# Kernel optimization log

Measured on AMD Instinct MI355X. Metric: run time of the kernel, lower is better.

## Reference

```python
import jax, jax.numpy as jnp
import numpy as np
import math

B, T, D_MODEL, N_HEAD = 2, 2048, 1024, 16
NUM_BUCKETS, MAX_DIST = 32, 128
D_HEAD = D_MODEL // N_HEAD


def _relative_position_bucket(rel_pos, num_buckets=NUM_BUCKETS, max_distance=MAX_DIST):
    # bidirectional=True branch of the torch code
    nb = num_buckets // 2
    buckets = (rel_pos > 0).astype(jnp.int32) * nb
    rel_pos = jnp.abs(rel_pos)
    max_exact = nb // 2
    is_small = rel_pos < max_exact
    # guard log(0); masked out by is_small anyway
    large = max_exact + (
        jnp.log(jnp.maximum(rel_pos, 1).astype(jnp.float32) / max_exact)
        / math.log(max_distance / max_exact) * (nb - max_exact)
    ).astype(jnp.int32)
    large = jnp.minimum(large, nb - 1)
    return buckets + jnp.where(is_small, rel_pos, large)


def compute_bias(rel_bias, q_len, kv_len):
    qp = jnp.arange(q_len, dtype=jnp.int32)[:, None]
    kp = jnp.arange(kv_len, dtype=jnp.int32)[None, :]
    buckets = _relative_position_bucket(kp - qp)          # [Tq, Tkv]
    vals = rel_bias[buckets]                              # [Tq, Tkv, H]
    return jnp.transpose(vals, (2, 0, 1))                 # [H, Tq, Tkv]


def setup_inputs() -> dict:
    key = jax.random.key(0)
    ks = jax.random.split(key, 9)
    inp = {
        'q': jax.random.normal(ks[0], (B, T, D_MODEL), jnp.float32),
        'k': jax.random.normal(ks[1], (B, T, D_MODEL), jnp.float32),
        'v': jax.random.normal(ks[2], (B, T, D_MODEL), jnp.float32),
        'mask': jax.random.randint(ks[3], (B, T, T), 0, 2, jnp.int32),
        'Wq': jax.random.normal(ks[4], (D_MODEL, D_MODEL), jnp.float32) * 0.02,
        'Wk': jax.random.normal(ks[5], (D_MODEL, D_MODEL), jnp.float32) * 0.02,
        'Wv': jax.random.normal(ks[6], (D_MODEL, D_MODEL), jnp.float32) * 0.02,
        'Wfc': jax.random.normal(ks[7], (D_MODEL, D_MODEL), jnp.float32) * 0.02,
        'rel_bias': jax.random.normal(ks[8], (NUM_BUCKETS, N_HEAD), jnp.float32) * 0.02,
    }
    return inp


def reference(q, k, v, mask, Wq, Wk, Wv, Wfc, rel_bias):
    b, tq, _ = q.shape
    tkv = k.shape[1]
    qh = (q @ Wq).reshape(b, tq, N_HEAD, D_HEAD)
    kh = (k @ Wk).reshape(b, tkv, N_HEAD, D_HEAD)
    vh = (v @ Wv).reshape(b, tkv, N_HEAD, D_HEAD)
    attn = jnp.einsum('blhd,bthd->bhlt', qh, kh) / np.sqrt(D_HEAD).astype(np.float32)
    position_bias = compute_bias(rel_bias, tq, tkv)       # [H, Tq, Tkv]
    attn = attn + position_bias[None]                     # broadcast over batch
    attn = jnp.where(mask[:, None] == 0, -1e9, attn)
    attn = jax.nn.softmax(attn, axis=-1)                  # dropout: eval mode (identity)
    out = jnp.einsum('bhlt,bthd->blhd', attn, vh).reshape(b, tq, D_MODEL)
    out = out @ Wfc
    return out, position_bias[:, None]                    # bias returned as [H,1,Tq,Tkv] like torch
```

## Files before the change

kernel.cpp:

```cpp
#include <hip/hip_runtime.h>
#include <math.h>

#define TT 2048
#define BB 2
#define HH 16
#define DMODEL 1024
#define NREL 4095

typedef __attribute__((ext_vector_type(8)))  _Float16 half8;
typedef __attribute__((ext_vector_type(4)))  _Float16 half4;
typedef __attribute__((ext_vector_type(16))) float    f32x16;
typedef __attribute__((ext_vector_type(4)))  int      int4v;

#define EXP2F(x) __builtin_amdgcn_exp2f(x)

__device__ __forceinline__ f32x16 zero16() {
    f32x16 v;
#pragma unroll
    for (int i = 0; i < 16; ++i) v[i] = 0.f;
    return v;
}

__device__ __forceinline__ unsigned pkh(float a, float b) {
    union { _Float16 h[2]; unsigned u; } x;
    x.h[0] = (_Float16)a; x.h[1] = (_Float16)b;
    return x.u;
}

__device__ __forceinline__ void gload16(const void* g, void* l) {
    __builtin_amdgcn_global_load_lds(
        (const __attribute__((address_space(1))) void*)g,
        (__attribute__((address_space(3))) void*)l, 16, 0, 0);
}

__device__ __forceinline__ int rel_bucket(int rel) {
    int base = rel > 0 ? 16 : 0;
    int r = rel < 0 ? -rel : rel;
    int lb;
    if (r < 8)       lb = r;
    else if (r < 12) lb = 8;
    else if (r < 16) lb = 9;
    else if (r < 23) lb = 10;
    else if (r < 32) lb = 11;
    else if (r < 46) lb = 12;
    else if (r < 64) lb = 13;
    else if (r < 91) lb = 14;
    else             lb = 15;
    return base + lb;
}

__global__ __launch_bounds__(256) void prep_kernel(
    const float* __restrict__ q, const float* __restrict__ k,
    const float* __restrict__ v, const int* __restrict__ mask,
    const float* __restrict__ W0, const float* __restrict__ W1,
    const float* __restrict__ W2, const float* __restrict__ W3,
    const float* __restrict__ rel_bias,
    _Float16* __restrict__ q16, _Float16* __restrict__ k16,
    _Float16* __restrict__ v16, _Float16* __restrict__ WT,
    float* __restrict__ btable, unsigned* __restrict__ mb)
{
    __shared__ float t[64][65];
    int bid = blockIdx.x, tid = threadIdx.x;
    if (bid < 256) {
        int idx = bid * 256 + tid;
        if (idx < HH * NREL) {
            int h = idx / NREL, ri = idx % NREL;
            btable[idx] = rel_bias[rel_bucket(ri - (TT - 1)) * HH + h];
        }
    } else if (bid < 1280) {
        int zz = (bid - 256) >> 8, inner = (bid - 256) & 255;
        const float* src = zz == 0 ? W0 : zz == 1 ? W1 : zz == 2 ? W2 : W3;
        _Float16* dst = WT + (size_t)zz * DMODEL * DMODEL;
        int k0 = (inner >> 4) * 64, n0 = (inner & 15) * 64;
        int r = tid >> 4, c4 = (tid & 15) * 4;
#pragma unroll
        for (int i = 0; i < 4; ++i) {
            float4 vv = *(const float4*)(src + (size_t)(k0 + r + 16 * i) * DMODEL + n0 + c4);
            t[r + 16 * i][c4] = vv.x; t[r + 16 * i][c4 + 1] = vv.y;
            t[r + 16 * i][c4 + 2] = vv.z; t[r + 16 * i][c4 + 3] = vv.w;
        }
        __syncthreads();
        int rn = tid >> 2, ck = (tid & 3) * 16;
        half8 h0, h1;
#pragma unroll
        for (int j = 0; j < 8; ++j) h0[j] = (_Float16)t[ck + j][rn];
#pragma unroll
        for (int j = 0; j < 8; ++j) h1[j] = (_Float16)t[ck + 8 + j][rn];
        *(half8*)(dst + (size_t)(n0 + rn) * DMODEL + k0 + ck) = h0;
        *(half8*)(dst + (size_t)(n0 + rn) * DMODEL + k0 + ck + 8) = h1;
    } else if (bid < 7424) {
        int zz = (bid - 1280) >> 11, inner = (bid - 1280) & 2047;
        const float* src = zz == 0 ? q : zz == 1 ? k : v;
        _Float16* dst = zz == 0 ? q16 : zz == 1 ? k16 : v16;
        int i = inner * 256 + tid;
        const float4* in4 = (const float4*)src;
        float4 v0 = in4[(size_t)i * 2], v1 = in4[(size_t)i * 2 + 1];
        half8 h = {(_Float16)v0.x, (_Float16)v0.y, (_Float16)v0.z, (_Float16)v0.w,
                   (_Float16)v1.x, (_Float16)v1.y, (_Float16)v1.z, (_Float16)v1.w};
        *(half8*)(dst + (size_t)i * 8) = h;
    } else {
        int g = (bid - 7424) * 256 + tid;
        int vv = mask[g];
        unsigned long long bal = __ballot(vv != 0);
        if ((g & 63) == 0) {
            int word = g >> 5;
            mb[word]     = (unsigned)bal;
            mb[word + 1] = (unsigned)(bal >> 32);
        }
    }
}

__global__ __launch_bounds__(256) void gemm_proj3(
    const _Float16* __restrict__ q16, const _Float16* __restrict__ k16,
    const _Float16* __restrict__ v16, const _Float16* __restrict__ WT,
    _Float16* __restrict__ qhf, _Float16* __restrict__ khf,
    _Float16* __restrict__ vtf, int zbase)
{
    __shared__ __align__(16) char lds[65536];
    int z = zbase + blockIdx.z;
    const _Float16* A  = z == 0 ? q16 : z == 1 ? k16 : v16;
    const _Float16* Bt = WT + (size_t)z * DMODEL * DMODEL;
    int bm = blockIdx.x * 128, bn = blockIdx.y * 128;
    int tid = threadIdx.x;
    int wv = tid >> 6, lane = tid & 63, hi = lane >> 5;
    int lo = lane & 31;
    int wr = wv >> 1, wc = wv & 1;
    int srow = wv * 32 + (lane >> 3);
    int scol = (lane & 7) * 8;
    const _Float16* Abase = A  + (size_t)(bm + srow) * DMODEL + scol;
    const _Float16* Bbase = Bt + (size_t)(bn + srow) * DMODEL + scol;

    f32x16 acc[2][2];
    acc[0][0] = zero16(); acc[0][1] = zero16();
    acc[1][0] = zero16(); acc[1][1] = zero16();

    auto stage = [&](int buf, int kt) {
#pragma unroll
        for (int t = 0; t < 4; ++t) {
            gload16(Abase + (size_t)t * 8 * DMODEL + kt * 64, lds + buf + wv * 4096 + t * 1024);
            gload16(Bbase + (size_t)t * 8 * DMODEL + kt * 64, lds + buf + 16384 + wv * 4096 + t * 1024);
        }
    };
    auto compute = [&](int buf) {
#pragma unroll
        for (int kk = 0; kk < 4; ++kk) {
            int cs = 2 * kk + hi;
            half8 a[2], b[2];
#pragma unroll
            for (int i = 0; i < 2; ++i) {
                a[i] = *(const half8*)(lds + buf + (wr * 64 + i * 32 + lo) * 128 + cs * 16);
                b[i] = *(const half8*)(lds + buf + 16384 + (wc * 64 + i * 32 + lo) * 128 + cs * 16);
            }
            acc[0][0] = __builtin_amdgcn_mfma_f32_32x32x16_f16(a[0], b[0], acc[0][0], 0, 0, 0);
            acc[0][1] = __builtin_amdgcn_mfma_f32_32x32x16_f16(a[0], b[1], acc[0][1], 0, 0, 0);
            acc[1][0] = __builtin_amdgcn_mfma_f32_32x32x16_f16(a[1], b[0], acc[1][0], 0, 0, 0);
            acc[1][1] = __builtin_amdgcn_mfma_f32_32x32x16_f16(a[1], b[1], acc[1][1], 0, 0, 0);
        }
    };

    stage(0, 0);
    __syncthreads();
    for (int kt = 0; kt < 16; kt += 2) {
        stage(32768, kt + 1);
        compute(0);
        __syncthreads();
        stage(0, kt + 2 < 16 ? kt + 2 : 15);
        compute(32768);
        __syncthreads();
    }

    if (z < 2) {
        _Float16* C = z == 0 ? qhf : khf;
#pragma unroll
        for (int j = 0; j < 2; ++j) {
            int n = bn + wc * 64 + j * 32 + lo;
            int h = n >> 6, d = n & 63;
#pragma unroll
            for (int i = 0; i < 2; ++i) {
                int mb2 = bm + wr * 64 + i * 32 + 4 * hi;
#pragma unroll
                for (int r = 0; r < 16; ++r) {
                    int m = mb2 + (r & 3) + 8 * (r >> 2);
                    int b = m >> 11, t = m & (TT - 1);
                    C[((size_t)(b * HH + h) * TT + t) * 64 + d] = (_Float16)acc[i][j][r];
                }
            }
        }
    } else {
#pragma unroll
        for (int j = 0; j < 2; ++j) {
            int n = bn + wc * 64 + j * 32 + lo;
            int h = n >> 6, d = n & 63;
#pragma unroll
            for (int i = 0; i < 2; ++i) {
                int mb2 = bm + wr * 64 + i * 32 + 4 * hi;
                int b = mb2 >> 11, tb = mb2 & (TT - 1);
#pragma unroll
                for (int r4 = 0; r4 < 4; ++r4) {
                    half4 hv = {(_Float16)acc[i][j][4 * r4 + 0], (_Float16)acc[i][j][4 * r4 + 1],
                                (_Float16)acc[i][j][4 * r4 + 2], (_Float16)acc[i][j][4 * r4 + 3]};
                    *(half4*)(vtf + ((size_t)(b * HH + h) * 64 + d) * TT + tb + 8 * r4) = hv;
                }
            }
        }
    }
}

__global__ __launch_bounds__(256) void attn_mfma(
    const _Float16* __restrict__ qh, const _Float16* __restrict__ kh,
    const _Float16* __restrict__ vt, const unsigned* __restrict__ maskbits,
    const float* __restrict__ btable, _Float16* __restrict__ Oout)
{
    __shared__ float bias_lds[4096];
    int bid = blockIdx.x;
    int xcd = bid & 7, j = bid >> 3;
    int qt = j & 15, bh = xcd + 8 * (j >> 4);
    int h = bh & 15, b = bh >> 4;
    int tid = threadIdx.x;
    int wv = tid >> 6, lane = tid & 63, lo = lane & 31, hi = lane >> 5;
    int q0 = qt * 128 + wv * 32;

    {
        const float* bsrc = btable + h * NREL;
#pragma unroll
        for (int i = 0; i < 16; ++i) {
            int idx = i * 256 + tid;
            bias_lds[idx] = bsrc[idx < NREL ? idx : NREL - 1] * 1.44269504f;
        }
    }

    const size_t bhoff = (size_t)(b * HH + h);
    const _Float16* Q = qh + (bhoff * TT + q0) * 64;
    const _Float16* K = kh + bhoff * TT * 64;
    const _Float16* V = vt + bhoff * 64 * TT;

    half8 qf[4];
#pragma unroll
    for (int c = 0; c < 4; ++c)
        qf[c] = *(const half8*)(Q + (size_t)lo * 64 + c * 16 + hi * 8);

    const int bofs = (TT - 1) - (q0 + lo) + 4 * hi;
    const unsigned* mw = maskbits + ((size_t)b * TT + q0 + lo) * 64;
    const float SC = 0.125f * 1.44269504f;

    f32x16 acco0 = zero16(), acco1 = zero16();
    float m = -INFINITY, l = 0.f;

    __syncthreads();

    for (int kt = 0; kt < 16; ++kt) {
        int k0 = kt * 128;
        unsigned wmA0 = mw[4 * kt], wmA1 = mw[4 * kt + 1];
        unsigned wmB0 = mw[4 * kt + 2], wmB1 = mw[4 * kt + 3];

        f32x16 sA0 = zero16(), sA1 = zero16(), sB0 = zero16(), sB1 = zero16();
        {
            half8 kf[4];
#pragma unroll
            for (int c = 0; c < 4; ++c)
                kf[c] = *(const half8*)(K + (size_t)(k0 + lo) * 64 + c * 16 + hi * 8);
            __builtin_amdgcn_s_setprio(1);
#pragma unroll
            for (int c = 0; c < 4; ++c)
                sA0 = __builtin_amdgcn_mfma_f32_32x32x16_f16(kf[c], qf[c], sA0, 0, 0, 0);
            __builtin_amdgcn_s_setprio(0);
#pragma unroll
            for (int c = 0; c < 4; ++c)
                kf[c] = *(const half8*)(K + (size_t)(k0 + 32 + lo) * 64 + c * 16 + hi * 8);
            __builtin_amdgcn_s_setprio(1);
#pragma unroll
            for (int c = 0; c < 4; ++c)
                sA1 = __builtin_amdgcn_mfma_f32_32x32x16_f16(kf[c], qf[c], sA1, 0, 0, 0);
            __builtin_amdgcn_s_setprio(0);
#pragma unroll
            for (int c = 0; c < 4; ++c)
                kf[c] = *(const half8*)(K + (size_t)(k0 + 64 + lo) * 64 + c * 16 + hi * 8);
            __builtin_amdgcn_s_setprio(1);
#pragma unroll
            for (int c = 0; c < 4; ++c)
                sB0 = __builtin_amdgcn_mfma_f32_32x32x16_f16(kf[c], qf[c], sB0, 0, 0, 0);
            __builtin_amdgcn_s_setprio(0);
#pragma unroll
            for (int c = 0; c < 4; ++c)
                kf[c] = *(const half8*)(K + (size_t)(k0 + 96 + lo) * 64 + c * 16 + hi * 8);
            __builtin_amdgcn_s_setprio(1);
#pragma unroll
            for (int c = 0; c < 4; ++c)
                sB1 = __builtin_amdgcn_mfma_f32_32x32x16_f16(kf[c], qf[c], sB1, 0, 0, 0);
            __builtin_amdgcn_s_setprio(0);
        }

        unsigned wsA0 = wmA0 >> (hi * 4), wsA1 = wmA1 >> (hi * 4);
        unsigned wsB0 = wmB0 >> (hi * 4), wsB1 = wmB1 >> (hi * 4);
        int bbase = bofs + k0;
#pragma unroll
        for (int r = 0; r < 16; ++r) {
            int sh = (r & 3) + 8 * (r >> 2);
            float a0 = fmaf(sA0[r], SC, bias_lds[bbase + sh]);
            float a1 = fmaf(sA1[r], SC, bias_lds[bbase + sh + 32]);
            float b0 = fmaf(sB0[r], SC, bias_lds[bbase + sh + 64]);
            float b1 = fmaf(sB1[r], SC, bias_lds[bbase + sh + 96]);
            sA0[r] = ((wsA0 >> sh) & 1) ? a0 : -1e9f;
            sA1[r] = ((wsA1 >> sh) & 1) ? a1 : -1e9f;
            sB0[r] = ((wsB0 >> sh) & 1) ? b0 : -1e9f;
            sB1[r] = ((wsB1 >> sh) & 1) ? b1 : -1e9f;
        }

        float tr[8];
#pragma unroll
        for (int r = 0; r < 8; ++r) {
            float x0 = fmaxf(fmaxf(sA0[r], sA0[r + 8]), fmaxf(sA1[r], sA1[r + 8]));
            float x1 = fmaxf(fmaxf(sB0[r], sB0[r + 8]), fmaxf(sB1[r], sB1[r + 8]));
            tr[r] = fmaxf(x0, x1);
        }
#pragma unroll
        for (int r = 0; r < 4; ++r) tr[r] = fmaxf(tr[r], tr[r + 4]);
        float tm = fmaxf(fmaxf(tr[0], tr[1]), fmaxf(tr[2], tr[3]));
        tm = fmaxf(tm, __shfl_xor(tm, 32));
        float mnew = fmaxf(m, tm);
        float corr = EXP2F(m - mnew);
        m = mnew;

#pragma unroll
        for (int r = 0; r < 16; ++r) sA0[r] = EXP2F(sA0[r] - m);
#pragma unroll
        for (int r = 0; r < 16; ++r) sA1[r] = EXP2F(sA1[r] - m);
#pragma unroll
        for (int r = 0; r < 16; ++r) sB0[r] = EXP2F(sB0[r] - m);
#pragma unroll
        for (int r = 0; r < 16; ++r) sB1[r] = EXP2F(sB1[r] - m);
#pragma unroll
        for (int r = 0; r < 8; ++r)
            tr[r] = ((sA0[r] + sA0[r + 8]) + (sA1[r] + sA1[r + 8]))
                  + ((sB0[r] + sB0[r + 8]) + (sB1[r] + sB1[r + 8]));
#pragma unroll
        for (int r = 0; r < 4; ++r) tr[r] += tr[r + 4];
        float rs = (tr[0] + tr[1]) + (tr[2] + tr[3]);
        rs += __shfl_xor(rs, 32);
        l = l * corr + rs;
#pragma unroll
        for (int r = 0; r < 16; ++r) { acco0[r] *= corr; acco1[r] *= corr; }

        half8 pbA[4], pbB[4];
#pragma unroll
        for (int g = 0; g < 2; ++g)
#pragma unroll
            for (int hc = 0; hc < 2; ++hc) {
                int r0 = hc * 8;
                float p0 = g ? sA1[r0 + 0] : sA0[r0 + 0];
                float p1 = g ? sA1[r0 + 1] : sA0[r0 + 1];
                float p2 = g ? sA1[r0 + 2] : sA0[r0 + 2];
                float p3 = g ? sA1[r0 + 3] : sA0[r0 + 3];
                float p4 = g ? sA1[r0 + 4] : sA0[r0 + 4];
                float p5 = g ? sA1[r0 + 5] : sA0[r0 + 5];
                float p6 = g ? sA1[r0 + 6] : sA0[r0 + 6];
                float p7 = g ? sA1[r0 + 7] : sA0[r0 + 7];
                unsigned w0 = pkh(p0, p1);
                unsigned w2 = pkh(p4, p5);
                asm("v_permlane32_swap_b32 %0, %1" : "+v"(w0), "+v"(w2));
                unsigned w1 = pkh(p2, p3);
                unsigned w3 = pkh(p6, p7);
                asm("v_permlane32_swap_b32 %0, %1" : "+v"(w1), "+v"(w3));
                union { int4v i; half8 hf; } cv;
                cv.i = (int4v){(int)w0, (int)w1, (int)w2, (int)w3};
                pbA[2 * g + hc] = cv.hf;
            }
#pragma unroll
        for (int g = 0; g < 2; ++g)
#pragma unroll
            for (int hc = 0; hc < 2; ++hc) {
                int r0 = hc * 8;
                float p0 = g ? sB1[r0 + 0] : sB0[r0 + 0];
                float p1 = g ? sB1[r0 + 1] : sB0[r0 + 1];
                float p2 = g ? sB1[r0 + 2] : sB0[r0 + 2];
                float p3 = g ? sB1[r0 + 3] : sB0[r0 + 3];
                float p4 = g ? sB1[r0 + 4] : sB0[r0 + 4];
                float p5 = g ? sB1[r0 + 5] : sB0[r0 + 5];
                float p6 = g ? sB1[r0 + 6] : sB0[r0 + 6];
                float p7 = g ? sB1[r0 + 7] : sB0[r0 + 7];
                unsigned w0 = pkh(p0, p1);
                unsigned w2 = pkh(p4, p5);
                asm("v_permlane32_swap_b32 %0, %1" : "+v"(w0), "+v"(w2));
                unsigned w1 = pkh(p2, p3);
                unsigned w3 = pkh(p6, p7);
                asm("v_permlane32_swap_b32 %0, %1" : "+v"(w1), "+v"(w3));
                union { int4v i; half8 hf; } cv;
                cv.i = (int4v){(int)w0, (int)w1, (int)w2, (int)w3};
                pbB[2 * g + hc] = cv.hf;
            }

        {
            half8 vf[4];
#pragma unroll
            for (int c = 0; c < 4; ++c)
                vf[c] = *(const half8*)(V + (size_t)lo * TT + k0 + c * 16 + hi * 8);
            __builtin_amdgcn_s_setprio(1);
#pragma unroll
            for (int c = 0; c < 4; ++c)
                acco0 = __builtin_amdgcn_mfma_f32_32x32x16_f16(vf[c], pbA[c], acco0, 0, 0, 0);
            __builtin_amdgcn_s_setprio(0);
#pragma unroll
            for (int c = 0; c < 4; ++c)
                vf[c] = *(const half8*)(V + (size_t)lo * TT + k0 + 64 + c * 16 + hi * 8);
            __builtin_amdgcn_s_setprio(1);
#pragma unroll
            for (int c = 0; c < 4; ++c)
                acco0 = __builtin_amdgcn_mfma_f32_32x32x16_f16(vf[c], pbB[c], acco0, 0, 0, 0);
            __builtin_amdgcn_s_setprio(0);
#pragma unroll
            for (int c = 0; c < 4; ++c)
                vf[c] = *(const half8*)(V + (size_t)(32 + lo) * TT + k0 + c * 16 + hi * 8);
            __builtin_amdgcn_s_setprio(1);
#pragma unroll
            for (int c = 0; c < 4; ++c)
                acco1 = __builtin_amdgcn_mfma_f32_32x32x16_f16(vf[c], pbA[c], acco1, 0, 0, 0);
            __builtin_amdgcn_s_setprio(0);
#pragma unroll
            for (int c = 0; c < 4; ++c)
                vf[c] = *(const half8*)(V + (size_t)(32 + lo) * TT + k0 + 64 + c * 16 + hi * 8);
            __builtin_amdgcn_s_setprio(1);
#pragma unroll
            for (int c = 0; c < 4; ++c)
                acco1 = __builtin_amdgcn_mfma_f32_32x32x16_f16(vf[c], pbB[c], acco1, 0, 0, 0);
            __builtin_amdgcn_s_setprio(0);
        }
    }

    float inv = 1.f / l;
    _Float16* op = Oout + (bhoff * TT + q0 + lo) * 64;
#pragma unroll
    for (int r4 = 0; r4 < 4; ++r4) {
        int d0 = 8 * r4 + 4 * hi;
        half4 h0 = {(_Float16)(acco0[4 * r4 + 0] * inv), (_Float16)(acco0[4 * r4 + 1] * inv),
                    (_Float16)(acco0[4 * r4 + 2] * inv), (_Float16)(acco0[4 * r4 + 3] * inv)};
        *(half4*)(op + d0) = h0;
        half4 h1 = {(_Float16)(acco1[4 * r4 + 0] * inv), (_Float16)(acco1[4 * r4 + 1] * inv),
                    (_Float16)(acco1[4 * r4 + 2] * inv), (_Float16)(acco1[4 * r4 + 3] * inv)};
        *(half4*)(op + d0 + 32) = h1;
    }
}

__global__ __launch_bounds__(256) void fc_bias_kernel(
    const _Float16* __restrict__ O, const _Float16* __restrict__ Bt,
    float* __restrict__ out0, const float* __restrict__ btable,
    float* __restrict__ out1)
{
    __shared__ __align__(16) char lds[65536];
    int bid = blockIdx.x, tid = threadIdx.x;
    if (bid >= 256) {
        const int n4 = HH * TT * TT / 4, stride = 2048 * 256;
        for (int i4 = (bid - 256) * 256 + tid; i4 < n4; i4 += stride) {
            int i = i4 * 4;
            int kk = i & (TT - 1);
            int qq = (i >> 11) & (TT - 1);
            int hh2 = i >> 22;
            const float* btp = btable + hh2 * NREL + (kk - qq + (TT - 1));
            float4 vv = make_float4(btp[0], btp[1], btp[2], btp[3]);
            reinterpret_cast<float4*>(out1)[i4] = vv;
        }
        return;
    }
    int bm = (bid & 31) * 128, bn = (bid >> 5) * 128;
    int wv = tid >> 6, lane = tid & 63, lo = lane & 31, hi = lane >> 5;
    int wr = wv >> 1, wc = wv & 1;
    int srow = wv * 32 + (lane >> 3);
    int scol = (lane & 7) * 8;
    int bb = bm >> 11, tbase = bm & (TT - 1);
    const _Float16* Abase = O + ((size_t)(bb * HH) * TT + tbase + srow) * 64 + scol;
    const _Float16* Bbase = Bt + (size_t)(bn + srow) * DMODEL + scol;

    f32x16 acc[2][2];
    acc[0][0] = zero16(); acc[0][1] = zero16();
    acc[1][0] = zero16(); acc[1][1] = zero16();

    auto stage = [&](int buf, int kt) {
#pragma unroll
        for (int t = 0; t < 4; ++t) {
            gload16(Abase + (size_t)kt * TT * 64 + (size_t)t * 8 * 64, lds + buf + wv * 4096 + t * 1024);
            gload16(Bbase + (size_t)t * 8 * DMODEL + kt * 64, lds + buf + 16384 + wv * 4096 + t * 1024);
        }
    };
    auto compute = [&](int buf) {
#pragma unroll
        for (int kk = 0; kk < 4; ++kk) {
            int cs = 2 * kk + hi;
            half8 a[2], b[2];
#pragma unroll
            for (int i = 0; i < 2; ++i) {
                a[i] = *(const half8*)(lds + buf + (wr * 64 + i * 32 + lo) * 128 + cs * 16);
                b[i] = *(const half8*)(lds + buf + 16384 + (wc * 64 + i * 32 + lo) * 128 + cs * 16);
            }
            acc[0][0] = __builtin_amdgcn_mfma_f32_32x32x16_f16(a[0], b[0], acc[0][0], 0, 0, 0);
            acc[0][1] = __builtin_amdgcn_mfma_f32_32x32x16_f16(a[0], b[1], acc[0][1], 0, 0, 0);
            acc[1][0] = __builtin_amdgcn_mfma_f32_32x32x16_f16(a[1], b[0], acc[1][0], 0, 0, 0);
            acc[1][1] = __builtin_amdgcn_mfma_f32_32x32x16_f16(a[1], b[1], acc[1][1], 0, 0, 0);
        }
    };

    stage(0, 0);
    __syncthreads();
    for (int kt = 0; kt < 16; kt += 2) {
        stage(32768, kt + 1);
        compute(0);
        __syncthreads();
        stage(0, kt + 2 < 16 ? kt + 2 : 15);
        compute(32768);
        __syncthreads();
    }

#pragma unroll
    for (int j = 0; j < 2; ++j) {
        int n = bn + wc * 64 + j * 32 + lo;
#pragma unroll
        for (int i = 0; i < 2; ++i) {
            int mb2 = bm + wr * 64 + i * 32 + 4 * hi;
#pragma unroll
            for (int r = 0; r < 16; ++r) {
                int m = mb2 + (r & 3) + 8 * (r >> 2);
                out0[(size_t)m * DMODEL + n] = acc[i][j][r];
            }
        }
    }
}

extern "C" void kernel_launch(void* const* d_in, const int* in_sizes, int n_in,
                              void* d_out, int out_size, void* d_ws, size_t ws_size,
                              hipStream_t stream) {
    const float* q        = (const float*)d_in[0];
    const float* k        = (const float*)d_in[1];
    const float* v        = (const float*)d_in[2];
    const int*   mask     = (const int*)  d_in[3];
    const float* Wq       = (const float*)d_in[4];
    const float* Wk       = (const float*)d_in[5];
    const float* Wv       = (const float*)d_in[6];
    const float* Wfc      = (const float*)d_in[7];
    const float* rel_bias = (const float*)d_in[8];

    float* out0 = (float*)d_out;
    float* out1 = out0 + (size_t)BB * TT * DMODEL;

    char* w = (char*)d_ws;
    _Float16* q16 = (_Float16*)(w);
    _Float16* k16 = (_Float16*)(w + ((size_t)8  << 20));
    _Float16* v16 = (_Float16*)(w + ((size_t)16 << 20));
    _Float16* qhf = (_Float16*)(w + ((size_t)24 << 20));
    _Float16* khf = (_Float16*)(w + ((size_t)32 << 20));
    _Float16* WT  = (_Float16*)(w + ((size_t)40 << 20));
    float*    btable = (float*)(w + ((size_t)48 << 20));
    unsigned* mbits  = (unsigned*)(w + ((size_t)48 << 20) + ((size_t)1 << 19));
    bool big = ws_size >= ((size_t)58 << 20);
    _Float16* vtf = big ? (_Float16*)(w + ((size_t)49 << 20) + ((size_t)1 << 19))
                        : k16;
    _Float16* O = v16;

    prep_kernel<<<dim3(40192), dim3(256), 0, stream>>>(
        q, k, v, mask, Wq, Wk, Wv, Wfc, rel_bias, q16, k16, v16, WT, btable, mbits);

    if (big) {
        gemm_proj3<<<dim3(32, 8, 3), dim3(256), 0, stream>>>(q16, k16, v16, WT,
                                                             qhf, khf, vtf, 0);
    } else {
        gemm_proj3<<<dim3(32, 8, 1), dim3(256), 0, stream>>>(q16, k16, v16, WT, qhf, khf, vtf, 0);
        gemm_proj3<<<dim3(32, 8, 1), dim3(256), 0, stream>>>(q16, k16, v16, WT, qhf, khf, vtf, 1);
        gemm_proj3<<<dim3(32, 8, 1), dim3(256), 0, stream>>>(q16, k16, v16, WT, qhf, khf, vtf, 2);
    }

    attn_mfma<<<dim3(BB * HH * 16), dim3(256), 0, stream>>>(
        qhf, khf, vtf, mbits, btable, O);

    fc_bias_kernel<<<dim3(2304), dim3(256), 0, stream>>>(
        O, WT + (size_t)3 * DMODEL * DMODEL, out0, btable, out1);
}
```

Measured before the change: 281.3 us.

## Fuse fp32-to-fp16 input conversion into projection GEMM A-tile staging

Drops the separate prep pass that cast q, k and v to fp16 in workspace. The projection GEMM now loads fp32 A tiles into registers, converts them and writes fp16 to LDS, while the B tiles still go through async global-to-LDS loads. This saves one full read and write round trip of the activations. In exchange it adds register pressure, VALU conversion work and synchronous loads inside the GEMM main loop, and the A-tile reads from global memory are twice as wide in bytes per tile.

```diff
diff --git a/kernel.cpp b/kernel.cpp
--- a/kernel.cpp
+++ b/kernel.cpp
@@ -50,13 +50,11 @@
 }
 
 __global__ __launch_bounds__(256) void prep_kernel(
-    const float* __restrict__ q, const float* __restrict__ k,
-    const float* __restrict__ v, const int* __restrict__ mask,
+    const int* __restrict__ mask,
     const float* __restrict__ W0, const float* __restrict__ W1,
     const float* __restrict__ W2, const float* __restrict__ W3,
     const float* __restrict__ rel_bias,
-    _Float16* __restrict__ q16, _Float16* __restrict__ k16,
-    _Float16* __restrict__ v16, _Float16* __restrict__ WT,
+    _Float16* __restrict__ WT,
     float* __restrict__ btable, unsigned* __restrict__ mb)
 {
     __shared__ float t[64][65];
@@ -88,18 +86,8 @@
         for (int j = 0; j < 8; ++j) h1[j] = (_Float16)t[ck + 8 + j][rn];
         *(half8*)(dst + (size_t)(n0 + rn) * DMODEL + k0 + ck) = h0;
         *(half8*)(dst + (size_t)(n0 + rn) * DMODEL + k0 + ck + 8) = h1;
-    } else if (bid < 7424) {
-        int zz = (bid - 1280) >> 11, inner = (bid - 1280) & 2047;
-        const float* src = zz == 0 ? q : zz == 1 ? k : v;
-        _Float16* dst = zz == 0 ? q16 : zz == 1 ? k16 : v16;
-        int i = inner * 256 + tid;
-        const float4* in4 = (const float4*)src;
-        float4 v0 = in4[(size_t)i * 2], v1 = in4[(size_t)i * 2 + 1];
-        half8 h = {(_Float16)v0.x, (_Float16)v0.y, (_Float16)v0.z, (_Float16)v0.w,
-                   (_Float16)v1.x, (_Float16)v1.y, (_Float16)v1.z, (_Float16)v1.w};
-        *(half8*)(dst + (size_t)i * 8) = h;
     } else {
-        int g = (bid - 7424) * 256 + tid;
+        int g = (bid - 1280) * 256 + tid;
         int vv = mask[g];
         unsigned long long bal = __ballot(vv != 0);
         if ((g & 63) == 0) {
@@ -111,14 +99,14 @@
 }
 
 __global__ __launch_bounds__(256) void gemm_proj3(
-    const _Float16* __restrict__ q16, const _Float16* __restrict__ k16,
-    const _Float16* __restrict__ v16, const _Float16* __restrict__ WT,
+    const float* __restrict__ qf32, const float* __restrict__ kf32,
+    const float* __restrict__ vf32, const _Float16* __restrict__ WT,
     _Float16* __restrict__ qhf, _Float16* __restrict__ khf,
     _Float16* __restrict__ vtf, int zbase)
 {
     __shared__ __align__(16) char lds[65536];
     int z = zbase + blockIdx.z;
-    const _Float16* A  = z == 0 ? q16 : z == 1 ? k16 : v16;
+    const float* A = z == 0 ? qf32 : z == 1 ? kf32 : vf32;
     const _Float16* Bt = WT + (size_t)z * DMODEL * DMODEL;
     int bm = blockIdx.x * 128, bn = blockIdx.y * 128;
     int tid = threadIdx.x;
@@ -127,18 +115,34 @@
     int wr = wv >> 1, wc = wv & 1;
     int srow = wv * 32 + (lane >> 3);
     int scol = (lane & 7) * 8;
-    const _Float16* Abase = A  + (size_t)(bm + srow) * DMODEL + scol;
+    const float*    Abase = A  + (size_t)(bm + srow) * DMODEL + scol;
     const _Float16* Bbase = Bt + (size_t)(bn + srow) * DMODEL + scol;
+    int awoff = wv * 4096 + (lane >> 3) * 128 + (lane & 7) * 16;
 
     f32x16 acc[2][2];
     acc[0][0] = zero16(); acc[0][1] = zero16();
     acc[1][0] = zero16(); acc[1][1] = zero16();
 
-    auto stage = [&](int buf, int kt) {
+    float4 ra[8];
+    auto loadA = [&](int kt) {
 #pragma unroll
         for (int t = 0; t < 4; ++t) {
-            gload16(Abase + (size_t)t * 8 * DMODEL + kt * 64, lds + buf + wv * 4096 + t * 1024);
+            ra[2 * t]     = *(const float4*)(Abase + (size_t)t * 8 * DMODEL + kt * 64);
+            ra[2 * t + 1] = *(const float4*)(Abase + (size_t)t * 8 * DMODEL + kt * 64 + 4);
+        }
+    };
+    auto gloadB = [&](int buf, int kt) {
+#pragma unroll
+        for (int t = 0; t < 4; ++t)
             gload16(Bbase + (size_t)t * 8 * DMODEL + kt * 64, lds + buf + 16384 + wv * 4096 + t * 1024);
+    };
+    auto writeA = [&](int buf) {
+#pragma unroll
+        for (int t = 0; t < 4; ++t) {
+            float4 v0 = ra[2 * t], v1 = ra[2 * t + 1];
+            half8 h = {(_Float16)v0.x, (_Float16)v0.y, (_Float16)v0.z, (_Float16)v0.w,
+                       (_Float16)v1.x, (_Float16)v1.y, (_Float16)v1.z, (_Float16)v1.w};
+            *(half8*)(lds + buf + awoff + t * 1024) = h;
         }
     };
     auto compute = [&](int buf) {
@@ -158,14 +162,16 @@
         }
     };
 
-    stage(0, 0);
+    loadA(0); gloadB(0, 0); writeA(0);
     __syncthreads();
     for (int kt = 0; kt < 16; kt += 2) {
-        stage(32768, kt + 1);
+        loadA(kt + 1); gloadB(32768, kt + 1);
         compute(0);
+        writeA(32768);
         __syncthreads();
-        stage(0, kt + 2 < 16 ? kt + 2 : 15);
+        if (kt + 2 < 16) { loadA(kt + 2); gloadB(0, kt + 2); }
         compute(32768);
+        if (kt + 2 < 16) writeA(0);
         __syncthreads();
     }
 
@@ -540,9 +546,7 @@
     float* out1 = out0 + (size_t)BB * TT * DMODEL;
 
     char* w = (char*)d_ws;
-    _Float16* q16 = (_Float16*)(w);
-    _Float16* k16 = (_Float16*)(w + ((size_t)8  << 20));
-    _Float16* v16 = (_Float16*)(w + ((size_t)16 << 20));
+    _Float16* O   = (_Float16*)(w);
     _Float16* qhf = (_Float16*)(w + ((size_t)24 << 20));
     _Float16* khf = (_Float16*)(w + ((size_t)32 << 20));
     _Float16* WT  = (_Float16*)(w + ((size_t)40 << 20));
@@ -550,19 +554,18 @@
     unsigned* mbits  = (unsigned*)(w + ((size_t)48 << 20) + ((size_t)1 << 19));
     bool big = ws_size >= ((size_t)58 << 20);
     _Float16* vtf = big ? (_Float16*)(w + ((size_t)49 << 20) + ((size_t)1 << 19))
-                        : k16;
-    _Float16* O = v16;
-
-    prep_kernel<<<dim3(40192), dim3(256), 0, stream>>>(
-        q, k, v, mask, Wq, Wk, Wv, Wfc, rel_bias, q16, k16, v16, WT, btable, mbits);
+                        : (_Float16*)(w + ((size_t)8 << 20));
+
+    prep_kernel<<<dim3(1280 + BB * TT * TT / 256), dim3(256), 0, stream>>>(
+        mask, Wq, Wk, Wv, Wfc, rel_bias, WT, btable, mbits);
 
     if (big) {
-        gemm_proj3<<<dim3(32, 8, 3), dim3(256), 0, stream>>>(q16, k16, v16, WT,
+        gemm_proj3<<<dim3(32, 8, 3), dim3(256), 0, stream>>>(q, k, v, WT,
                                                              qhf, khf, vtf, 0);
     } else {
-        gemm_proj3<<<dim3(32, 8, 1), dim3(256), 0, stream>>>(q16, k16, v16, WT, qhf, khf, vtf, 0);
-        gemm_proj3<<<dim3(32, 8, 1), dim3(256), 0, stream>>>(q16, k16, v16, WT, qhf, khf, vtf, 1);
-        gemm_proj3<<<dim3(32, 8, 1), dim3(256), 0, stream>>>(q16, k16, v16, WT, qhf, khf, vtf, 2);
+        gemm_proj3<<<dim3(32, 8, 1), dim3(256), 0, stream>>>(q, k, v, WT, qhf, khf, vtf, 0);
+        gemm_proj3<<<dim3(32, 8, 1), dim3(256), 0, stream>>>(q, k, v, WT, qhf, khf, vtf, 1);
+        gemm_proj3<<<dim3(32, 8, 1), dim3(256), 0, stream>>>(q, k, v, WT, qhf, khf, vtf, 2);
     }
 
     attn_mfma<<<dim3(BB * HH * 16), dim3(256), 0, stream>>>(
```

Measured after the change: 282.5 us. Within noise of the previous version (+0.4%).
